# Performance work log

Hardware: AMD Instinct MI355X
Metric: run time of the kernel (lower is better)

## Reference

```python
import jax, jax.numpy as jnp
import numpy as np

INPUT_DIM = 512
PROJ_DIM = 128
HIDDEN = INPUT_DIM // 2  # 256


def setup_inputs() -> dict:
    key = jax.random.key(0)
    ks = jax.random.split(key, 6)
    B = 8192
    s1 = 1.0 / np.sqrt(INPUT_DIM)
    s2 = 1.0 / np.sqrt(HIDDEN)
    return {
        "fused_text": jax.random.normal(ks[0], (B, INPUT_DIM), dtype=jnp.float32),
        "x": jax.random.normal(ks[1], (B, INPUT_DIM), dtype=jnp.float32),
        # generator layer 1: Linear(input_dim, input_dim//2), torch layout [out, in]
        "W1": jax.random.uniform(ks[2], (HIDDEN, INPUT_DIM), jnp.float32, -s1, s1),
        "b1": jax.random.uniform(ks[3], (HIDDEN,), jnp.float32, -s1, s1),
        # generator layer 2: Linear(input_dim//2, proj_dim * input_dim)
        "W2": jax.random.uniform(ks[4], (PROJ_DIM * INPUT_DIM, HIDDEN), jnp.float32, -s2, s2),
        "b2": jax.random.uniform(ks[5], (PROJ_DIM * INPUT_DIM,), jnp.float32, -s2, s2),
    }


def reference(fused_text, x, W1, b1, W2, b2):
    B = fused_text.shape[0]
    # hypernetwork generator MLP
    h = jax.nn.relu(fused_text @ W1.T + b1)          # [B, hidden]
    w_flat = h @ W2.T + b2                           # [B, proj_dim * input_dim]
    W = w_flat.reshape(B, PROJ_DIM, INPUT_DIM)       # per-sample weights
    # per-sample projection: bmm(W, x[..., None]).squeeze(-1)
    out = jnp.einsum("bpi,bi->bp", W, x)             # [B, proj_dim]
    return out
```

## Files before the change

### kernel.cpp

```cpp
#include <hip/hip_runtime.h>
#include <stdint.h>

#define B_SZ   8192
#define IN_DIM 512
#define HID    256
#define PROJ   128

typedef __attribute__((ext_vector_type(8))) short bf16x8;
typedef __attribute__((ext_vector_type(4))) float f32x4;

#define GLDS16(gp, lp) __builtin_amdgcn_global_load_lds( \
    (const __attribute__((address_space(1))) void*)(gp), \
    (__attribute__((address_space(3))) void*)(lp), 16, 0, 0)

__device__ __forceinline__ unsigned short f2bf(float f) {
    union { float f; uint32_t u; } c; c.f = f;
    uint32_t u = c.u;
    uint32_t r = (u + 0x7fffu + ((u >> 16) & 1u)) >> 16;
    return (unsigned short)r;
}
__device__ __forceinline__ float bfhi(uint32_t v) {
    union { uint32_t u; float f; } c; c.u = v & 0xffff0000u; return c.f;
}
__device__ __forceinline__ float bflo(uint32_t v) {
    union { uint32_t u; float f; } c; c.u = v << 16; return c.f;
}

__global__ __launch_bounds__(256) void k0_prep(
        const float4* __restrict__ W2, ushort4* __restrict__ W2b,
        const float* __restrict__ x, unsigned short* __restrict__ xTb) {
    __shared__ float tile[64][65];
    const int bid = blockIdx.x;
    if (bid < 2048) {
        const int nW2 = (PROJ * IN_DIM * HID) / 4;
        const int stride = 2048 * 256;
        for (int i = bid * 256 + threadIdx.x; i < nW2; i += stride) {
            float4 v = W2[i];
            ushort4 o;
            o.x = f2bf(v.x); o.y = f2bf(v.y); o.z = f2bf(v.z); o.w = f2bf(v.w);
            W2b[i] = o;
        }
    } else {
        const int tb = bid - 2048;
        const int bi = tb & 7, bb = tb >> 3;
        const int i0 = bi * 64, b0 = bb * 64;
        const int t = threadIdx.x;
        const int c = t & 63, r4 = t >> 6;
        #pragma unroll
        for (int rr = 0; rr < 64; rr += 4)
            tile[rr + r4][c] = x[(size_t)(b0 + rr + r4) * IN_DIM + i0 + c];
        __syncthreads();
        #pragma unroll
        for (int rr = 0; rr < 64; rr += 4)
            xTb[(size_t)(i0 + rr + r4) * B_SZ + b0 + c] = f2bf(tile[c][rr + r4]);
    }
}

__device__ __forceinline__ bf16x8 ld_cvt8(const float* __restrict__ s) {
    float4 a = *(const float4*)s;
    float4 b = *(const float4*)(s + 4);
    bf16x8 r;
    r[0] = (short)f2bf(a.x); r[1] = (short)f2bf(a.y);
    r[2] = (short)f2bf(a.z); r[3] = (short)f2bf(a.w);
    r[4] = (short)f2bf(b.x); r[5] = (short)f2bf(b.y);
    r[6] = (short)f2bf(b.z); r[7] = (short)f2bf(b.w);
    return r;
}

__global__ __launch_bounds__(256) void k1_hidden(
        const float* __restrict__ ft,
        const float* __restrict__ W1,
        const float* __restrict__ b1,
        unsigned short* __restrict__ hb) {
    const int lane = threadIdx.x & 63;
    const int wv   = threadIdx.x >> 6;
    const int l15  = lane & 15, q = lane >> 4;
    const int b0 = blockIdx.x * 64;
    const int n0 = wv * 64;

    f32x4 acc[4][4];
    const f32x4 z4 = {0.f, 0.f, 0.f, 0.f};
    #pragma unroll
    for (int mt = 0; mt < 4; ++mt)
        #pragma unroll
        for (int nt = 0; nt < 4; ++nt) acc[mt][nt] = z4;

    for (int kq = 0; kq < 16; ++kq) {
        const int koff = kq * 32 + q * 8;
        bf16x8 a[4], bb[4];
        #pragma unroll
        for (int mt = 0; mt < 4; ++mt)
            a[mt] = ld_cvt8(ft + (size_t)(b0 + mt*16 + l15) * IN_DIM + koff);
        #pragma unroll
        for (int nt = 0; nt < 4; ++nt)
            bb[nt] = ld_cvt8(W1 + (size_t)(n0 + nt*16 + l15) * IN_DIM + koff);
        #pragma unroll
        for (int mt = 0; mt < 4; ++mt)
            #pragma unroll
            for (int nt = 0; nt < 4; ++nt)
                acc[mt][nt] = __builtin_amdgcn_mfma_f32_16x16x32_bf16(
                    a[mt], bb[nt], acc[mt][nt], 0, 0, 0);
    }
    #pragma unroll
    for (int nt = 0; nt < 4; ++nt) {
        float bias = b1[n0 + nt*16 + l15];
        #pragma unroll
        for (int mt = 0; mt < 4; ++mt)
            #pragma unroll
            for (int r = 0; r < 4; ++r) {
                float v = acc[mt][nt][r] + bias;
                v = fmaxf(v, 0.f);
                hb[(size_t)(b0 + mt*16 + q*4 + r) * HID + n0 + nt*16 + l15] = f2bf(v);
            }
    }
}

__global__ __launch_bounds__(256, 3) void k3_main(
        const unsigned short* __restrict__ W2b,
        const unsigned short* __restrict__ hb,
        const unsigned short* __restrict__ xTb,
        const float* __restrict__ b2,
        float* __restrict__ out) {
    __shared__ unsigned short lbs[2][8192];
    const int tid  = threadIdx.x;
    const int lane = tid & 63;
    const int wv   = tid >> 6;
    const int l15  = lane & 15, q = lane >> 4;
    const int pgrp = blockIdx.x & 63;
    const int bsup = blockIdx.x >> 6;
    const int p0   = pgrp * 2;
    const int b0w  = bsup * 256 + wv * 64;
    const f32x4 z4 = {0.f, 0.f, 0.f, 0.f};

    const unsigned short* wrowbase =
        W2b + ((size_t)(p0 + (wv >> 1)) * IN_DIM + (wv & 1) * 16 + l15) * HID + q * 8;

    float oacc[2][4][4];
    #pragma unroll
    for (int pp = 0; pp < 2; ++pp)
        #pragma unroll
        for (int mt = 0; mt < 4; ++mt)
            #pragma unroll
            for (int r = 0; r < 4; ++r) oacc[pp][mt][r] = 0.f;

    bf16x8 afr[4][4];

    {
        unsigned short* Ld = &lbs[0][wv * 2048];
        #pragma unroll
        for (int jj = 0; jj < 4; ++jj)
            GLDS16(wrowbase + jj * 32, Ld + jj * 512);
    }

    #pragma unroll 1
    for (int t = 0; t < 32; ++t) {
        __syncthreads();

        if (t < 31) {
            const int tn = t + 1;
            const int kh_n = tn >> 4, i0_n = (tn & 15) * 32;
            unsigned short* Ld = &lbs[tn & 1][wv * 2048];
            const unsigned short* gs = wrowbase + (size_t)i0_n * HID + kh_n * 128;
            #pragma unroll
            for (int jj = 0; jj < 4; ++jj)
                GLDS16(gs + jj * 32, Ld + jj * 512);
        }

        const int kh = t >> 4;
        if ((t & 15) == 0) {
            #pragma unroll
            for (int mt = 0; mt < 4; ++mt) {
                const unsigned short* hrow =
                    hb + (size_t)(b0w + mt*16 + l15) * HID + kh * 128 + q * 8;
                #pragma unroll
                for (int kq = 0; kq < 4; ++kq)
                    afr[mt][kq] = *(const bf16x8*)(hrow + kq * 32);
            }
        }

        const unsigned short* Lb = &lbs[t & 1][lane * 8];
        const int i0 = (t & 15) * 32;

        #pragma unroll
        for (int sub = 0; sub < 2; ++sub) {
            const int irow = i0 + sub * 16 + l15;
            uint2 xv[4];
            const unsigned short* xp = xTb + (size_t)irow * B_SZ + b0w + q * 4;
            #pragma unroll
            for (int mt = 0; mt < 4; ++mt)
                xv[mt] = *(const uint2*)(xp + mt * 16);

            float b2v = 0.f, b2w = 0.f;
            if (kh == 0) {
                b2v = b2[p0 * 512 + irow];
                b2w = b2[(p0 + 1) * 512 + irow];
            }

            #pragma unroll
            for (int pp = 0; pp < 2; ++pp) {
                bf16x8 bfr[4];
                #pragma unroll
                for (int kq = 0; kq < 4; ++kq)
                    bfr[kq] = *(const bf16x8*)(Lb + ((pp*2 + sub)*4 + kq) * 512);

                f32x4 D[4];
                #pragma unroll
                for (int mt = 0; mt < 4; ++mt)
                    D[mt] = __builtin_amdgcn_mfma_f32_16x16x32_bf16(afr[mt][0], bfr[0], z4, 0, 0, 0);
                #pragma unroll
                for (int kq = 1; kq < 4; ++kq)
                    #pragma unroll
                    for (int mt = 0; mt < 4; ++mt)
                        D[mt] = __builtin_amdgcn_mfma_f32_16x16x32_bf16(afr[mt][kq], bfr[kq], D[mt], 0, 0, 0);

                const float bb = pp ? b2w : b2v;
                #pragma unroll
                for (int mt = 0; mt < 4; ++mt) {
                    oacc[pp][mt][0] = fmaf(D[mt][0] + bb, bflo(xv[mt].x), oacc[pp][mt][0]);
                    oacc[pp][mt][1] = fmaf(D[mt][1] + bb, bfhi(xv[mt].x), oacc[pp][mt][1]);
                    oacc[pp][mt][2] = fmaf(D[mt][2] + bb, bflo(xv[mt].y), oacc[pp][mt][2]);
                    oacc[pp][mt][3] = fmaf(D[mt][3] + bb, bfhi(xv[mt].y), oacc[pp][mt][3]);
                }
            }
        }
    }

    #pragma unroll
    for (int pp = 0; pp < 2; ++pp)
        #pragma unroll
        for (int mt = 0; mt < 4; ++mt)
            #pragma unroll
            for (int r = 0; r < 4; ++r) {
                float v = oacc[pp][mt][r];
                v += __shfl_xor(v, 1, 16);
                v += __shfl_xor(v, 2, 16);
                v += __shfl_xor(v, 4, 16);
                v += __shfl_xor(v, 8, 16);
                if (l15 == 0)
                    out[(size_t)(b0w + mt*16 + q*4 + r) * PROJ + p0 + pp] = v;
            }
}

extern "C" void kernel_launch(void* const* d_in, const int* in_sizes, int n_in,
                              void* d_out, int out_size, void* d_ws, size_t ws_size,
                              hipStream_t stream) {
    const float* ft = (const float*)d_in[0];
    const float* x  = (const float*)d_in[1];
    const float* W1 = (const float*)d_in[2];
    const float* b1 = (const float*)d_in[3];
    const float* W2 = (const float*)d_in[4];
    const float* b2 = (const float*)d_in[5];
    float* out = (float*)d_out;

    char* ws = (char*)d_ws;
    unsigned short* W2b = (unsigned short*)(ws);
    unsigned short* hb  = (unsigned short*)(ws + 33554432);
    unsigned short* xTb = (unsigned short*)(ws + 37748736);

    hipLaunchKernelGGL(k0_prep, dim3(3072), dim3(256), 0, stream,
        (const float4*)W2, (ushort4*)W2b, x, xTb);
    hipLaunchKernelGGL(k1_hidden, dim3(128), dim3(256), 0, stream, ft, W1, b1, hb);
    hipLaunchKernelGGL(k3_main, dim3(2048), dim3(256), 0, stream, W2b, hb, xTb, b2, out);
}
```

Before: 551.3 us.

## Pre-swizzle bf16 W2 into per-tile contiguous layout for LDS loads

The W2 conversion kernel now writes bf16 W2 in a tile-major order matching how the main kernel consumes each 32-row by 128-k tile, so each wave's global-to-LDS loads read contiguous 512-element chunks. This replaces strided row gathers with sequential reads in the hot kernel. In exchange, the conversion step runs on only 128 blocks with a serial loop, which lowers parallelism in the prep phase, and the fragment indexing in LDS is remapped.

Result: no change. 560.4 us (+1.6%).

```diff
diff --git a/kernel.cpp b/kernel.cpp
--- a/kernel.cpp
+++ b/kernel.cpp
@@ -27,21 +27,39 @@
 }
 
 __global__ __launch_bounds__(256) void k0_prep(
-        const float4* __restrict__ W2, ushort4* __restrict__ W2b,
+        const float* __restrict__ W2, unsigned short* __restrict__ W2s,
         const float* __restrict__ x, unsigned short* __restrict__ xTb) {
     __shared__ float tile[64][65];
     const int bid = blockIdx.x;
-    if (bid < 2048) {
-        const int nW2 = (PROJ * IN_DIM * HID) / 4;
-        const int stride = 2048 * 256;
-        for (int i = bid * 256 + threadIdx.x; i < nW2; i += stride) {
-            float4 v = W2[i];
-            ushort4 o;
-            o.x = f2bf(v.x); o.y = f2bf(v.y); o.z = f2bf(v.z); o.w = f2bf(v.w);
-            W2b[i] = o;
+    if (bid < 128) {
+        const int p    = bid;
+        const int w    = threadIdx.x >> 6;
+        const int lane = threadIdx.x & 63;
+        const int q    = lane & 3;
+        const int l15  = lane >> 2;
+        const float* src_p = W2 + (size_t)p * 512 * HID;
+        unsigned short* dst_p = W2s + (size_t)p * 131072;
+        #pragma unroll 1
+        for (int t = 0; t < 32; ++t) {
+            const int kh = t >> 4, i0 = (t & 15) * 32;
+            #pragma unroll
+            for (int fi = 0; fi < 2; ++fi) {
+                const int f   = w + fi * 4;
+                const int sub = f >> 2, kq = f & 3;
+                const float* s = src_p
+                    + (size_t)(i0 + sub*16 + l15) * HID + kh*128 + kq*32 + q*8;
+                float4 a = *(const float4*)s;
+                float4 b = *(const float4*)(s + 4);
+                ushort4 o1, o2;
+                o1.x = f2bf(a.x); o1.y = f2bf(a.y); o1.z = f2bf(a.z); o1.w = f2bf(a.w);
+                o2.x = f2bf(b.x); o2.y = f2bf(b.y); o2.z = f2bf(b.z); o2.w = f2bf(b.w);
+                unsigned short* d = dst_p + t*4096 + f*512 + (q*16 + l15)*8;
+                *(ushort4*)d = o1;
+                *(ushort4*)(d + 4) = o2;
+            }
         }
     } else {
-        const int tb = bid - 2048;
+        const int tb = bid - 128;
         const int bi = tb & 7, bb = tb >> 3;
         const int i0 = bi * 64, b0 = bb * 64;
         const int t = threadIdx.x;
@@ -116,7 +134,7 @@
 }
 
 __global__ __launch_bounds__(256, 3) void k3_main(
-        const unsigned short* __restrict__ W2b,
+        const unsigned short* __restrict__ W2s,
         const unsigned short* __restrict__ hb,
         const unsigned short* __restrict__ xTb,
         const float* __restrict__ b2,
@@ -132,8 +150,11 @@
     const int b0w  = bsup * 256 + wv * 64;
     const f32x4 z4 = {0.f, 0.f, 0.f, 0.f};
 
-    const unsigned short* wrowbase =
-        W2b + ((size_t)(p0 + (wv >> 1)) * IN_DIM + (wv & 1) * 16 + l15) * HID + q * 8;
+    const int spp  = wv >> 1;
+    const int g0   = (wv & 1) * 4;
+    const unsigned short* wsrc =
+        W2s + (size_t)(p0 + spp) * 131072 + lane * 8;
+    const int ldst0 = (spp * 8 + g0) * 512;
 
     float oacc[2][4][4];
     #pragma unroll
@@ -145,12 +166,9 @@
 
     bf16x8 afr[4][4];
 
-    {
-        unsigned short* Ld = &lbs[0][wv * 2048];
-        #pragma unroll
-        for (int jj = 0; jj < 4; ++jj)
-            GLDS16(wrowbase + jj * 32, Ld + jj * 512);
-    }
+    #pragma unroll
+    for (int jj = 0; jj < 4; ++jj)
+        GLDS16(wsrc + (g0 + jj) * 512, &lbs[0][ldst0 + jj * 512]);
 
     #pragma unroll 1
     for (int t = 0; t < 32; ++t) {
@@ -158,12 +176,11 @@
 
         if (t < 31) {
             const int tn = t + 1;
-            const int kh_n = tn >> 4, i0_n = (tn & 15) * 32;
-            unsigned short* Ld = &lbs[tn & 1][wv * 2048];
-            const unsigned short* gs = wrowbase + (size_t)i0_n * HID + kh_n * 128;
+            unsigned short* Ld = &lbs[tn & 1][ldst0];
+            const unsigned short* gs = wsrc + tn * 4096 + g0 * 512;
             #pragma unroll
             for (int jj = 0; jj < 4; ++jj)
-                GLDS16(gs + jj * 32, Ld + jj * 512);
+                GLDS16(gs + jj * 512, Ld + jj * 512);
         }
 
         const int kh = t >> 4;
@@ -201,7 +218,7 @@
                 bf16x8 bfr[4];
                 #pragma unroll
                 for (int kq = 0; kq < 4; ++kq)
-                    bfr[kq] = *(const bf16x8*)(Lb + ((pp*2 + sub)*4 + kq) * 512);
+                    bfr[kq] = *(const bf16x8*)(Lb + ((pp*8 + sub*4) + kq) * 512);
 
                 f32x4 D[4];
                 #pragma unroll
@@ -253,12 +270,12 @@
     float* out = (float*)d_out;
 
     char* ws = (char*)d_ws;
-    unsigned short* W2b = (unsigned short*)(ws);
+    unsigned short* W2s = (unsigned short*)(ws);
     unsigned short* hb  = (unsigned short*)(ws + 33554432);
     unsigned short* xTb = (unsigned short*)(ws + 37748736);
 
-    hipLaunchKernelGGL(k0_prep, dim3(3072), dim3(256), 0, stream,
-        (const float4*)W2, (ushort4*)W2b, x, xTb);
+    hipLaunchKernelGGL(k0_prep, dim3(1152), dim3(256), 0, stream,
+        W2, W2s, x, xTb);
     hipLaunchKernelGGL(k1_hidden, dim3(128), dim3(256), 0, stream, ft, W1, b1, hb);
-    hipLaunchKernelGGL(k3_main, dim3(2048), dim3(256), 0, stream, W2b, hb, xTb, b2, out);
-}
+    hipLaunchKernelGGL(k3_main, dim3(2048), dim3(256), 0, stream, W2s, hb, xTb, b2, out);
+}
```
